# Optimization experiments

Measured on AMD Instinct MI355X. Metric: run time of the kernel, lower is better.

Reference implementation:

```python
import jax, jax.numpy as jnp
import numpy as np

N = 100000
MUL = 16


def _build_cg():
    # Real-basis Clebsch-Gordan (Wigner-3j-style) coefficients, shape (2l1+1, 2l2+1, 2lo+1),
    # each normalized to unit Frobenius norm per output component (e3nn component normalization).
    eps = np.zeros((3, 3, 3), np.float32)
    for a, b, c in [(0, 1, 2), (1, 2, 0), (2, 0, 1)]:
        eps[a, b, c] = 1.0
        eps[a, c, b] = -1.0
    s2 = np.float32(1.0 / np.sqrt(2.0))
    q = np.zeros((5, 3, 3), np.float32)  # l=2 real harmonics: xy, yz, 3z^2-r^2, xz, x^2-y^2
    q[0, 0, 1] = q[0, 1, 0] = s2
    q[1, 1, 2] = q[1, 2, 1] = s2
    q[2] = np.diag([-1.0, -1.0, 2.0]).astype(np.float32) / np.sqrt(6.0)
    q[3, 0, 2] = q[3, 2, 0] = s2
    q[4] = np.diag([1.0, -1.0, 0.0]).astype(np.float32) * s2
    cg000 = jnp.ones((1, 1, 1), jnp.float32)                                   # 0e x 0e -> 0e
    cg011 = jnp.asarray(np.eye(3, dtype=np.float32)[None])                      # 0e x 1o -> 1o
    cg110 = jnp.asarray((np.eye(3, dtype=np.float32) / np.sqrt(3.0))[:, :, None])  # 1o x 1o -> 0e
    cg111 = jnp.asarray(eps * s2)                                               # 1o x 1o -> 1e
    cg112 = jnp.asarray(np.transpose(q, (1, 2, 0)))                             # 1o x 1o -> 2e
    return cg000, cg011, cg110, cg111, cg112


def _path(x1, x2, cg, w, alpha):
    # 'uvw' tensor-product path: out[z,w,m] = alpha * sum_{u,v,i,j} x1[z,u,i] x2[z,v,j] cg[i,j,m] w[u,v,w]
    # Contraction order chosen to keep the largest intermediate at [z,u,w,j].
    t = jnp.einsum('zvj,uvw->zuwj', x2, w)
    s = jnp.einsum('zui,zuwj->zwij', x1, t)
    return alpha * jnp.einsum('zwij,ijm->zwm', s, cg)


def _tensor_square(x, w0, w1, w2, w3, w4):
    n = x.shape[0]
    x0 = x[:, :MUL].reshape(n, MUL, 1)       # 16x0e
    x1 = x[:, MUL:].reshape(n, MUL, 3)       # 16x1o
    cg000, cg011, cg110, cg111, cg112 = _build_cg()
    a2 = 1.0 / np.sqrt(MUL * MUL * 2.0)      # 0e output receives 2 paths
    a1 = 1.0 / np.sqrt(MUL * MUL * 1.0)
    o_0e = _path(x0, x0, cg000, w0, a2) + _path(x1, x1, cg110, w2, a2)
    o_1o = _path(x0, x1, cg011, w1, a1)
    o_1e = _path(x1, x1, cg111, w3, a1)
    o_2e = _path(x1, x1, cg112, w4, a1)
    return jnp.concatenate([o.reshape(n, -1) for o in (o_0e, o_1o, o_1e, o_2e)], axis=1)


def setup_inputs() -> dict:
    key = jax.random.key(0)
    kx, k0, k1, k2, k3, k4 = jax.random.split(key, 6)
    return {
        'x': jax.random.normal(kx, (N, MUL * 1 + MUL * 3), jnp.float32),
        'w0': jax.random.normal(k0, (MUL, MUL, MUL), jnp.float32),
        'w1': jax.random.normal(k1, (MUL, MUL, MUL), jnp.float32),
        'w2': jax.random.normal(k2, (MUL, MUL, MUL), jnp.float32),
        'w3': jax.random.normal(k3, (MUL, MUL, MUL), jnp.float32),
        'w4': jax.random.normal(k4, (MUL, MUL, MUL), jnp.float32),
    }


def reference(x, w0, w1, w2, w3, w4):
    return _tensor_square(x, w0, w1, w2, w3, w4)
```

## Files before the change

### kernel.cpp

```cpp
#include <hip/hip_runtime.h>
#include <hip/hip_bf16.h>

typedef __attribute__((ext_vector_type(8))) short short8;
typedef __attribute__((ext_vector_type(4))) float float4v;
typedef __attribute__((ext_vector_type(2))) float float2v;
typedef __attribute__((ext_vector_type(4))) unsigned uint4v;

#define S_A 0.04419417382415922f
#define S_B 0.025515518153991442f
#define S_C 0.0625f

static __device__ __forceinline__ unsigned pkbf(float a, float b) {
#if __has_builtin(__builtin_amdgcn_cvt_pk_bf16_f32)
    auto v = __builtin_amdgcn_cvt_pk_bf16_f32(a, b);
    return __builtin_bit_cast(unsigned, v);
#else
    unsigned ua = __builtin_bit_cast(unsigned, a);
    unsigned ub = __builtin_bit_cast(unsigned, b);
    ua += 0x7fffu + ((ua >> 16) & 1u);
    ub += 0x7fffu + ((ub >> 16) & 1u);
    return __builtin_amdgcn_perm(ub, ua, 0x07060302);
#endif
}

__global__ void wprep_kernel(const float* __restrict__ wA, const float* __restrict__ wB,
                             const float* __restrict__ wC, const float* __restrict__ wD,
                             const float* __restrict__ wE, unsigned short* __restrict__ wout)
{
    int e = blockIdx.x * 256 + threadIdx.x;
    if (e >= 5 * 4096) return;
    int p = e >> 12;
    int rem = e & 4095;
    const float* wp = (p == 0) ? wA : (p == 1) ? wB : (p == 2) ? wC : (p == 3) ? wD : wE;
    unsigned u = __builtin_bit_cast(unsigned, wp[rem]);
    u += 0x7fffu + ((u >> 16) & 1u);
    int k = rem >> 4, w = rem & 15;
    int c = k >> 5, kk = k & 31;
    int lane = ((kk >> 3) << 4) | w;
    int j = kk & 7;
    wout[(((c * 5 + p) * 64 + lane) << 3) | j] = (unsigned short)(u >> 16);
}

template<int G>
static __device__ __forceinline__ void run_group(
    const float* __restrict__ xr, int l, const short8* __restrict__ wbase,
    float* __restrict__ out, long long z0)
{
    const int r  = l & 15;
    const int g  = l >> 4;
    const int v0 = (g & 1) * 8;
    const int uo = g >> 1;

    float2v Xv[4], Yv[4], Zv[4];
    float2v A0v[4];
    {
        float b[24];
        #pragma unroll
        for (int q = 0; q < 6; q++)
            *(float4v*)&b[q * 4] = *(const float4v*)(xr + 16 + v0 * 3 + q * 4);
        #pragma unroll
        for (int t = 0; t < 4; t++) {
            Xv[t] = (float2v){b[6 * t + 0], b[6 * t + 3]};
            Yv[t] = (float2v){b[6 * t + 1], b[6 * t + 4]};
            Zv[t] = (float2v){b[6 * t + 2], b[6 * t + 5]};
        }
        if constexpr (G == 1) {
            float a[8];
            #pragma unroll
            for (int q = 0; q < 2; q++)
                *(float4v*)&a[q * 4] = *(const float4v*)(xr + v0 + q * 4);
            #pragma unroll
            for (int t = 0; t < 4; t++) A0v[t] = (float2v){a[2 * t], a[2 * t + 1]};
        }
    }

    constexpr int NS = (G == 1) ? 4 : 3;
    float4v acc[NS];
    #pragma unroll
    for (int s = 0; s < NS; s++) acc[s] = (float4v){0.f, 0.f, 0.f, 0.f};

    #pragma unroll
    for (int c = 0; c < 8; c++) {
        short8 wfA, wfB, wfC;
        if constexpr (G == 0) wfA = wbase[(c * 5 + 2) * 64 + l];
        if constexpr (G == 1) {
            wfA = wbase[(c * 5 + 0) * 64 + l];
            wfB = wbase[(c * 5 + 1) * 64 + l];
            wfC = wbase[(c * 5 + 4) * 64 + l];
        }
        if constexpr (G == 2) wfA = wbase[(c * 5 + 3) * 64 + l];
        if constexpr (G == 3) wfA = wbase[(c * 5 + 4) * 64 + l];

        const int u = c * 2 + uo;
        float u0 = 0.f, ux = 0.f, uy = 0.f, uz = 0.f;
        if constexpr (G == 0 || G == 1) u0 = xr[u];
        if constexpr (G != 0) {
            ux = xr[16 + u * 3 + 0];
            uy = xr[16 + u * 3 + 1];
            uz = xr[16 + u * 3 + 2];
        }

        unsigned fri[NS][4];
        #pragma unroll
        for (int t = 0; t < 4; t++) {
            const float2v X = Xv[t], Y = Yv[t], Z = Zv[t];
            if constexpr (G == 0) {
                float2v b2 = u0 * X, b3 = u0 * Y, b4 = u0 * Z;
                fri[0][t] = pkbf(b2.x, b2.y);
                fri[1][t] = pkbf(b3.x, b3.y);
                fri[2][t] = pkbf(b4.x, b4.y);
            }
            if constexpr (G == 1) {
                float2v p00 = ux * X, p11 = uy * Y, p22 = uz * Z;
                float2v b0 = u0 * A0v[t];
                float2v b1 = p00 + p11 + p22;
                float2v b10 = 2.0f * p22 - p00 - p11;
                float2v b12 = p00 - p11;
                fri[0][t] = pkbf(b0.x, b0.y);
                fri[1][t] = pkbf(b1.x, b1.y);
                fri[2][t] = pkbf(b10.x, b10.y);
                fri[3][t] = pkbf(b12.x, b12.y);
            }
            if constexpr (G == 2) {
                float2v p01 = ux * Y, p02 = ux * Z, p10 = uy * X;
                float2v p12 = uy * Z, p20 = uz * X, p21 = uz * Y;
                float2v b5 = p12 - p21, b6 = p20 - p02, b7 = p01 - p10;
                fri[0][t] = pkbf(b5.x, b5.y);
                fri[1][t] = pkbf(b6.x, b6.y);
                fri[2][t] = pkbf(b7.x, b7.y);
            }
            if constexpr (G == 3) {
                float2v p01 = ux * Y, p02 = ux * Z, p10 = uy * X;
                float2v p12 = uy * Z, p20 = uz * X, p21 = uz * Y;
                float2v b8 = p01 + p10, b9 = p12 + p21, b11 = p02 + p20;
                fri[0][t] = pkbf(b8.x, b8.y);
                fri[1][t] = pkbf(b9.x, b9.y);
                fri[2][t] = pkbf(b11.x, b11.y);
            }
        }

        #pragma unroll
        for (int s = 0; s < NS; s++) {
            short8 frm = __builtin_bit_cast(short8, *(uint4v*)fri[s]);
            const short8& wf = (G == 1) ? ((s == 0) ? wfA : (s == 1) ? wfB : wfC) : wfA;
            acc[s] = __builtin_amdgcn_mfma_f32_16x16x32_bf16(frm, wf, acc[s], 0, 0, 0);
        }
    }

    const int w = r;
    float* outp = out + (z0 + g * 4) * 192;
    #pragma unroll
    for (int reg = 0; reg < 4; reg++) {
        float* rowp = outp + reg * 192;
        if constexpr (G == 0) {
            rowp[16 + w * 3 + 0] = S_C * acc[0][reg];
            rowp[16 + w * 3 + 1] = S_C * acc[1][reg];
            rowp[16 + w * 3 + 2] = S_C * acc[2][reg];
        }
        if constexpr (G == 1) {
            rowp[w]               = S_A * acc[0][reg] + S_B * acc[1][reg];
            rowp[112 + w * 5 + 2] = S_B * acc[2][reg];
            rowp[112 + w * 5 + 4] = S_A * acc[3][reg];
        }
        if constexpr (G == 2) {
            rowp[64 + w * 3 + 0] = S_A * acc[0][reg];
            rowp[64 + w * 3 + 1] = S_A * acc[1][reg];
            rowp[64 + w * 3 + 2] = S_A * acc[2][reg];
        }
        if constexpr (G == 3) {
            rowp[112 + w * 5 + 0] = S_A * acc[0][reg];
            rowp[112 + w * 5 + 1] = S_A * acc[1][reg];
            rowp[112 + w * 5 + 3] = S_A * acc[2][reg];
        }
    }
}

__global__ __launch_bounds__(256)
void tsq_kernel(const float* __restrict__ x,
                const unsigned short* __restrict__ wfrag,
                float* __restrict__ out,
                int nrows)
{
    __shared__ __attribute__((aligned(16))) float xlds[16 * 68];

    const int tid = threadIdx.x;
    const long long z0 = (long long)blockIdx.x * 16;

    {
        const float* xg = x + z0 * 64;
        int f = tid * 4;
        int row = f >> 6, col = f & 63;
        float4v v = {0.f, 0.f, 0.f, 0.f};
        if (z0 + row < nrows) v = *(const float4v*)(xg + f);
        *(float4v*)&xlds[row * 68 + col] = v;
    }
    __syncthreads();
    if (z0 >= nrows) return;

    const int wave = tid >> 6;
    const int l = tid & 63;
    const float* xr = &xlds[(l & 15) * 68];
    const short8* wbase = (const short8*)wfrag;

    if      (wave == 0) run_group<0>(xr, l, wbase, out, z0);
    else if (wave == 1) run_group<1>(xr, l, wbase, out, z0);
    else if (wave == 2) run_group<2>(xr, l, wbase, out, z0);
    else                run_group<3>(xr, l, wbase, out, z0);
}

extern "C" void kernel_launch(void* const* d_in, const int* in_sizes, int n_in,
                              void* d_out, int out_size, void* d_ws, size_t ws_size,
                              hipStream_t stream) {
    const float* x  = (const float*)d_in[0];
    const float* w0 = (const float*)d_in[1];
    const float* w1 = (const float*)d_in[2];
    const float* w2 = (const float*)d_in[3];
    const float* w3 = (const float*)d_in[4];
    const float* w4 = (const float*)d_in[5];
    float* out = (float*)d_out;
    unsigned short* wfrag = (unsigned short*)d_ws;
    (void)ws_size; (void)n_in; (void)out_size;

    const int nrows = in_sizes[0] / 64;
    const int nblocks = (nrows + 15) / 16;

    wprep_kernel<<<dim3(80), dim3(256), 0, stream>>>(w0, w2, w1, w3, w4, wfrag);
    tsq_kernel<<<dim3(nblocks), dim3(256), 0, stream>>>(x, wfrag, out, nrows);
}
```

Before: 137.4 us.

## Split path groups into single-wave blocks processing 32-row tiles

After: 161.2 us. 17.3% more time.

```diff
diff --git a/kernel.cpp b/kernel.cpp
--- a/kernel.cpp
+++ b/kernel.cpp
@@ -43,26 +43,31 @@
 
 template<int G>
 static __device__ __forceinline__ void run_group(
-    const float* __restrict__ xr, int l, const short8* __restrict__ wbase,
-    float* __restrict__ out, long long z0)
+    const float* __restrict__ xlds, int l, const short8* __restrict__ wbase,
+    float* __restrict__ out, long long z0, int nrows)
 {
     const int r  = l & 15;
     const int g  = l >> 4;
     const int v0 = (g & 1) * 8;
     const int uo = g >> 1;
 
-    float2v Xv[4], Yv[4], Zv[4];
-    float2v A0v[4];
-    {
+    const float* xr0 = xlds + r * 68;
+    const float* xr1 = xlds + (16 + r) * 68;
+
+    float2v Xv[2][4], Yv[2][4], Zv[2][4];
+    float2v A0v[2][4];
+    #pragma unroll
+    for (int T = 0; T < 2; T++) {
+        const float* xr = T ? xr1 : xr0;
         float b[24];
         #pragma unroll
         for (int q = 0; q < 6; q++)
             *(float4v*)&b[q * 4] = *(const float4v*)(xr + 16 + v0 * 3 + q * 4);
         #pragma unroll
         for (int t = 0; t < 4; t++) {
-            Xv[t] = (float2v){b[6 * t + 0], b[6 * t + 3]};
-            Yv[t] = (float2v){b[6 * t + 1], b[6 * t + 4]};
-            Zv[t] = (float2v){b[6 * t + 2], b[6 * t + 5]};
+            Xv[T][t] = (float2v){b[6 * t + 0], b[6 * t + 3]};
+            Yv[T][t] = (float2v){b[6 * t + 1], b[6 * t + 4]};
+            Zv[T][t] = (float2v){b[6 * t + 2], b[6 * t + 5]};
         }
         if constexpr (G == 1) {
             float a[8];
@@ -70,14 +75,16 @@
             for (int q = 0; q < 2; q++)
                 *(float4v*)&a[q * 4] = *(const float4v*)(xr + v0 + q * 4);
             #pragma unroll
-            for (int t = 0; t < 4; t++) A0v[t] = (float2v){a[2 * t], a[2 * t + 1]};
+            for (int t = 0; t < 4; t++) A0v[T][t] = (float2v){a[2 * t], a[2 * t + 1]};
         }
     }
 
     constexpr int NS = (G == 1) ? 4 : 3;
-    float4v acc[NS];
-    #pragma unroll
-    for (int s = 0; s < NS; s++) acc[s] = (float4v){0.f, 0.f, 0.f, 0.f};
+    float4v acc[2][NS];
+    #pragma unroll
+    for (int T = 0; T < 2; T++)
+        #pragma unroll
+        for (int s = 0; s < NS; s++) acc[T][s] = (float4v){0.f, 0.f, 0.f, 0.f};
 
     #pragma unroll
     for (int c = 0; c < 8; c++) {
@@ -92,120 +99,131 @@
         if constexpr (G == 3) wfA = wbase[(c * 5 + 4) * 64 + l];
 
         const int u = c * 2 + uo;
-        float u0 = 0.f, ux = 0.f, uy = 0.f, uz = 0.f;
-        if constexpr (G == 0 || G == 1) u0 = xr[u];
-        if constexpr (G != 0) {
-            ux = xr[16 + u * 3 + 0];
-            uy = xr[16 + u * 3 + 1];
-            uz = xr[16 + u * 3 + 2];
-        }
-
-        unsigned fri[NS][4];
-        #pragma unroll
-        for (int t = 0; t < 4; t++) {
-            const float2v X = Xv[t], Y = Yv[t], Z = Zv[t];
+
+        #pragma unroll
+        for (int T = 0; T < 2; T++) {
+            const float* xr = T ? xr1 : xr0;
+            float u0 = 0.f, ux = 0.f, uy = 0.f, uz = 0.f;
+            if constexpr (G == 0 || G == 1) u0 = xr[u];
+            if constexpr (G != 0) {
+                ux = xr[16 + u * 3 + 0];
+                uy = xr[16 + u * 3 + 1];
+                uz = xr[16 + u * 3 + 2];
+            }
+
+            unsigned fri[NS][4];
+            #pragma unroll
+            for (int t = 0; t < 4; t++) {
+                const float2v X = Xv[T][t], Y = Yv[T][t], Z = Zv[T][t];
+                if constexpr (G == 0) {
+                    float2v b2 = u0 * X, b3 = u0 * Y, b4 = u0 * Z;
+                    fri[0][t] = pkbf(b2.x, b2.y);
+                    fri[1][t] = pkbf(b3.x, b3.y);
+                    fri[2][t] = pkbf(b4.x, b4.y);
+                }
+                if constexpr (G == 1) {
+                    float2v p00 = ux * X, p11 = uy * Y, p22 = uz * Z;
+                    float2v b0 = u0 * A0v[T][t];
+                    float2v b1 = p00 + p11 + p22;
+                    float2v b10 = 2.0f * p22 - p00 - p11;
+                    float2v b12 = p00 - p11;
+                    fri[0][t] = pkbf(b0.x, b0.y);
+                    fri[1][t] = pkbf(b1.x, b1.y);
+                    fri[2][t] = pkbf(b10.x, b10.y);
+                    fri[3][t] = pkbf(b12.x, b12.y);
+                }
+                if constexpr (G == 2) {
+                    float2v p01 = ux * Y, p02 = ux * Z, p10 = uy * X;
+                    float2v p12 = uy * Z, p20 = uz * X, p21 = uz * Y;
+                    float2v b5 = p12 - p21, b6 = p20 - p02, b7 = p01 - p10;
+                    fri[0][t] = pkbf(b5.x, b5.y);
+                    fri[1][t] = pkbf(b6.x, b6.y);
+                    fri[2][t] = pkbf(b7.x, b7.y);
+                }
+                if constexpr (G == 3) {
+                    float2v p01 = ux * Y, p02 = ux * Z, p10 = uy * X;
+                    float2v p12 = uy * Z, p20 = uz * X, p21 = uz * Y;
+                    float2v b8 = p01 + p10, b9 = p12 + p21, b11 = p02 + p20;
+                    fri[0][t] = pkbf(b8.x, b8.y);
+                    fri[1][t] = pkbf(b9.x, b9.y);
+                    fri[2][t] = pkbf(b11.x, b11.y);
+                }
+            }
+
+            #pragma unroll
+            for (int s = 0; s < NS; s++) {
+                short8 frm = __builtin_bit_cast(short8, *(uint4v*)fri[s]);
+                const short8& wf = (G == 1) ? ((s == 0) ? wfA : (s == 1) ? wfB : wfC) : wfA;
+                acc[T][s] = __builtin_amdgcn_mfma_f32_16x16x32_bf16(frm, wf, acc[T][s], 0, 0, 0);
+            }
+        }
+    }
+
+    const int w = r;
+    #pragma unroll
+    for (int T = 0; T < 2; T++) {
+        float* outp = out + (z0 + T * 16 + g * 4) * 192;
+        #pragma unroll
+        for (int reg = 0; reg < 4; reg++) {
+            if (z0 + T * 16 + g * 4 + reg >= nrows) break;
+            float* rowp = outp + reg * 192;
             if constexpr (G == 0) {
-                float2v b2 = u0 * X, b3 = u0 * Y, b4 = u0 * Z;
-                fri[0][t] = pkbf(b2.x, b2.y);
-                fri[1][t] = pkbf(b3.x, b3.y);
-                fri[2][t] = pkbf(b4.x, b4.y);
+                rowp[16 + w * 3 + 0] = S_C * acc[T][0][reg];
+                rowp[16 + w * 3 + 1] = S_C * acc[T][1][reg];
+                rowp[16 + w * 3 + 2] = S_C * acc[T][2][reg];
             }
             if constexpr (G == 1) {
-                float2v p00 = ux * X, p11 = uy * Y, p22 = uz * Z;
-                float2v b0 = u0 * A0v[t];
-                float2v b1 = p00 + p11 + p22;
-                float2v b10 = 2.0f * p22 - p00 - p11;
-                float2v b12 = p00 - p11;
-                fri[0][t] = pkbf(b0.x, b0.y);
-                fri[1][t] = pkbf(b1.x, b1.y);
-                fri[2][t] = pkbf(b10.x, b10.y);
-                fri[3][t] = pkbf(b12.x, b12.y);
+                rowp[w]               = S_A * acc[T][0][reg] + S_B * acc[T][1][reg];
+                rowp[112 + w * 5 + 2] = S_B * acc[T][2][reg];
+                rowp[112 + w * 5 + 4] = S_A * acc[T][3][reg];
             }
             if constexpr (G == 2) {
-                float2v p01 = ux * Y, p02 = ux * Z, p10 = uy * X;
-                float2v p12 = uy * Z, p20 = uz * X, p21 = uz * Y;
-                float2v b5 = p12 - p21, b6 = p20 - p02, b7 = p01 - p10;
-                fri[0][t] = pkbf(b5.x, b5.y);
-                fri[1][t] = pkbf(b6.x, b6.y);
-                fri[2][t] = pkbf(b7.x, b7.y);
+                rowp[64 + w * 3 + 0] = S_A * acc[T][0][reg];
+                rowp[64 + w * 3 + 1] = S_A * acc[T][1][reg];
+                rowp[64 + w * 3 + 2] = S_A * acc[T][2][reg];
             }
             if constexpr (G == 3) {
-                float2v p01 = ux * Y, p02 = ux * Z, p10 = uy * X;
-                float2v p12 = uy * Z, p20 = uz * X, p21 = uz * Y;
-                float2v b8 = p01 + p10, b9 = p12 + p21, b11 = p02 + p20;
-                fri[0][t] = pkbf(b8.x, b8.y);
-                fri[1][t] = pkbf(b9.x, b9.y);
-                fri[2][t] = pkbf(b11.x, b11.y);
-            }
-        }
-
-        #pragma unroll
-        for (int s = 0; s < NS; s++) {
-            short8 frm = __builtin_bit_cast(short8, *(uint4v*)fri[s]);
-            const short8& wf = (G == 1) ? ((s == 0) ? wfA : (s == 1) ? wfB : wfC) : wfA;
-            acc[s] = __builtin_amdgcn_mfma_f32_16x16x32_bf16(frm, wf, acc[s], 0, 0, 0);
-        }
-    }
-
-    const int w = r;
-    float* outp = out + (z0 + g * 4) * 192;
-    #pragma unroll
-    for (int reg = 0; reg < 4; reg++) {
-        float* rowp = outp + reg * 192;
-        if constexpr (G == 0) {
-            rowp[16 + w * 3 + 0] = S_C * acc[0][reg];
-            rowp[16 + w * 3 + 1] = S_C * acc[1][reg];
-            rowp[16 + w * 3 + 2] = S_C * acc[2][reg];
-        }
-        if constexpr (G == 1) {
-            rowp[w]               = S_A * acc[0][reg] + S_B * acc[1][reg];
-            rowp[112 + w * 5 + 2] = S_B * acc[2][reg];
-            rowp[112 + w * 5 + 4] = S_A * acc[3][reg];
-        }
-        if constexpr (G == 2) {
-            rowp[64 + w * 3 + 0] = S_A * acc[0][reg];
-            rowp[64 + w * 3 + 1] = S_A * acc[1][reg];
-            rowp[64 + w * 3 + 2] = S_A * acc[2][reg];
-        }
-        if constexpr (G == 3) {
-            rowp[112 + w * 5 + 0] = S_A * acc[0][reg];
-            rowp[112 + w * 5 + 1] = S_A * acc[1][reg];
-            rowp[112 + w * 5 + 3] = S_A * acc[2][reg];
-        }
-    }
-}
-
-__global__ __launch_bounds__(256)
+                rowp[112 + w * 5 + 0] = S_A * acc[T][0][reg];
+                rowp[112 + w * 5 + 1] = S_A * acc[T][1][reg];
+                rowp[112 + w * 5 + 3] = S_A * acc[T][2][reg];
+            }
+        }
+    }
+}
+
+__global__ __launch_bounds__(64)
 void tsq_kernel(const float* __restrict__ x,
                 const unsigned short* __restrict__ wfrag,
                 float* __restrict__ out,
                 int nrows)
 {
-    __shared__ __attribute__((aligned(16))) float xlds[16 * 68];
-
-    const int tid = threadIdx.x;
-    const long long z0 = (long long)blockIdx.x * 16;
+    __shared__ __attribute__((aligned(16))) float xlds[32 * 68];
+
+    const int l = threadIdx.x;
+    const int bid = blockIdx.x;
+    const int grp = bid & 3;
+    const long long z0 = (long long)(bid >> 2) * 32;
 
     {
         const float* xg = x + z0 * 64;
-        int f = tid * 4;
-        int row = f >> 6, col = f & 63;
-        float4v v = {0.f, 0.f, 0.f, 0.f};
-        if (z0 + row < nrows) v = *(const float4v*)(xg + f);
-        *(float4v*)&xlds[row * 68 + col] = v;
+        #pragma unroll
+        for (int q = 0; q < 8; q++) {
+            int e = q * 64 + l;
+            int row = e >> 4, col = (e & 15) * 4;
+            float4v v = {0.f, 0.f, 0.f, 0.f};
+            if (z0 + row < nrows) v = *(const float4v*)(xg + e * 4);
+            *(float4v*)&xlds[row * 68 + col] = v;
+        }
     }
     __syncthreads();
     if (z0 >= nrows) return;
 
-    const int wave = tid >> 6;
-    const int l = tid & 63;
-    const float* xr = &xlds[(l & 15) * 68];
     const short8* wbase = (const short8*)wfrag;
 
-    if      (wave == 0) run_group<0>(xr, l, wbase, out, z0);
-    else if (wave == 1) run_group<1>(xr, l, wbase, out, z0);
-    else if (wave == 2) run_group<2>(xr, l, wbase, out, z0);
-    else                run_group<3>(xr, l, wbase, out, z0);
+    if      (grp == 0) run_group<0>(xlds, l, wbase, out, z0, nrows);
+    else if (grp == 1) run_group<1>(xlds, l, wbase, out, z0, nrows);
+    else if (grp == 2) run_group<2>(xlds, l, wbase, out, z0, nrows);
+    else               run_group<3>(xlds, l, wbase, out, z0, nrows);
 }
 
 extern "C" void kernel_launch(void* const* d_in, const int* in_sizes, int n_in,
@@ -222,8 +240,9 @@
     (void)ws_size; (void)n_in; (void)out_size;
 
     const int nrows = in_sizes[0] / 64;
-    const int nblocks = (nrows + 15) / 16;
+    const int ntiles = (nrows + 31) / 32;
+    const int nblocks = ntiles * 4;
 
     wprep_kernel<<<dim3(80), dim3(256), 0, stream>>>(w0, w2, w1, w3, w4, wfrag);
-    tsq_kernel<<<dim3(nblocks), dim3(256), 0, stream>>>(x, wfrag, out, nrows);
-}
+    tsq_kernel<<<dim3(nblocks), dim3(64), 0, stream>>>(x, wfrag, out, nrows);
+}
```
